# Kernel tuning notes

Hardware: AMD Instinct MI355X
Metric: run time of the kernel (lower is better)

## Reference

```python
import jax, jax.numpy as jnp
import numpy as np

DIM = 768
HEADS = 12
ROWS = COLS = 24          # 384 // 16
NP = ROWS * COLS          # 576 patches
N = NP + 1                # +1 cls token
NREL = (2 * ROWS - 1) * (2 * COLS - 1)  # 2209 relative offsets


def make_mapping_indices():
    # mapping[(di,dj)] = (di+ROWS-1)*(2*COLS-1) + (dj+COLS-1), vectorized
    i = np.arange(ROWS)[:, None, None, None]
    j = np.arange(COLS)[None, :, None, None]
    ii = np.arange(ROWS)[None, None, :, None]
    jj = np.arange(COLS)[None, None, None, :]
    idx = ((ii - i) + ROWS - 1) * (2 * COLS - 1) + ((jj - j) + COLS - 1)
    return jnp.asarray(idx.reshape(NP, NP), dtype=jnp.int32)


def setup_inputs() -> dict:
    key = jax.random.key(0)
    ks = jax.random.split(key, 7)
    B = 32
    x = jax.random.normal(ks[0], (B, N, DIM), dtype=jnp.float32)
    qkv_w = jax.random.normal(ks[1], (3 * DIM, DIM), dtype=jnp.float32) * 0.02
    proj_w = jax.random.normal(ks[2], (DIM, DIM), dtype=jnp.float32) * 0.02
    proj_b = jnp.zeros((DIM,), dtype=jnp.float32)
    beta1 = jax.random.normal(ks[3], (HEADS, 1, 1 + NP), dtype=jnp.float32) * 0.02
    beta2 = jax.random.normal(ks[4], (HEADS, NP, 1), dtype=jnp.float32) * 0.02
    beta3 = jax.random.normal(ks[5], (HEADS, NREL), dtype=jnp.float32) * 0.02
    return {"x": x, "qkv_w": qkv_w, "proj_w": proj_w, "proj_b": proj_b,
            "beta1": beta1, "beta2": beta2, "beta3": beta3,
            "mapping_indices": make_mapping_indices()}


def reference(x, qkv_w, proj_w, proj_b, beta1, beta2, beta3, mapping_indices):
    B, Nn, C = x.shape
    H = HEADS
    D = C // H
    scale = D ** -0.5
    qkv = x @ qkv_w.T                               # (B,N,3C)
    qkv = qkv.reshape(B, Nn, 3, H, D).transpose(2, 0, 3, 1, 4)
    q, k, v = qkv[0], qkv[1], qkv[2]                # (B,H,N,D)
    attn = jnp.einsum('bhid,bhjd->bhij', q, k) * scale
    # T5-style bias: (H, NP, NP) gathered rel bias + beta2 first col + beta1 last row
    rel = beta3[:, mapping_indices]                 # (H, NP, NP)
    top = jnp.concatenate([beta2, rel], axis=2)     # (H, NP, NP+1)
    beta_matrix = jnp.concatenate([top, beta1], axis=1)  # (H, N, N)
    attn = attn + beta_matrix[None]
    attn = jax.nn.softmax(attn, axis=-1)
    out = jnp.einsum('bhij,bhjd->bhid', attn, v)    # (B,H,N,D)
    out = out.transpose(0, 2, 1, 3).reshape(B, Nn, C)
    return out @ proj_w.T + proj_b
```

## Files before the change

kernel.cpp:

```cpp
#include <hip/hip_runtime.h>
#include <math.h>

#define DIMC  768
#define HEADS 12
#define NTOK  577
#define NPAT  576
#define NRELS 2209
#define BATCH 32
#define HDIM  64
#define MROWS (BATCH * NTOK)
#define NQB   5
#define NCH   10

#define AS1 __attribute__((address_space(1)))
#define AS3 __attribute__((address_space(3)))

typedef __attribute__((ext_vector_type(8))) short bf16x8;
typedef __attribute__((ext_vector_type(4))) float f32x4;
typedef __attribute__((ext_vector_type(8))) unsigned short u16x8;

__device__ __forceinline__ unsigned short f2bf(float f) {
    unsigned int u = __float_as_uint(f);
    return (unsigned short)((u + 0x7FFFu + ((u >> 16) & 1u)) >> 16);
}
__device__ __forceinline__ float bf2f(unsigned short h) {
    return __uint_as_float(((unsigned int)h) << 16);
}

__global__ __launch_bounds__(256)
void f32_to_bf16_kernel(const float* __restrict__ in, unsigned short* __restrict__ out, int n4) {
    for (int i = blockIdx.x * 256 + threadIdx.x; i < n4; i += gridDim.x * 256) {
        float4 v = reinterpret_cast<const float4*>(in)[i];
        ushort4 r;
        r.x = f2bf(v.x); r.y = f2bf(v.y); r.z = f2bf(v.z); r.w = f2bf(v.w);
        reinterpret_cast<ushort4*>(out)[i] = r;
    }
}

__global__ __launch_bounds__(256)
void build_biasF_kernel(const float* __restrict__ beta1,
                        const float* __restrict__ beta2,
                        const float* __restrict__ beta3,
                        unsigned short* __restrict__ biasF) {
    int idx = blockIdx.x * 256 + threadIdx.x;
    const int total = HEADS * NQB * NCH * 4 * 64 * 32;
    if (idx >= total) return;
    int r    = idx & 3;
    int bb   = (idx >> 2) & 3;
    int qi   = (idx >> 4) & 1;
    int lane = (idx >> 5) & 63;
    int wv   = (idx >> 11) & 3;
    int u    = idx >> 13;
    int c    = u % NCH;
    int i0b  = (u / NCH) % NQB;
    int h    = u / (NCH * NQB);
    int q = i0b * 128 + wv * 32 + qi * 16 + (lane & 15);
    int j = c * 64 + bb * 16 + ((lane >> 4) << 2) + r;
    float v;
    if (q >= NTOK || j >= NTOK) {
        v = -1e30f;
    } else if (q == NPAT) {
        v = beta1[h * NTOK + j];
    } else if (j == 0) {
        v = beta2[h * NPAT + q];
    } else {
        int p   = j - 1;
        int qi_ = q / 24, qj = q - qi_ * 24;
        int ri  = p / 24, ci = p - ri * 24;
        v = beta3[h * NRELS + (ri - qi_ + 23) * 47 + (ci - qj + 23)];
    }
    biasF[idx] = f2bf(v);
}

__global__ __launch_bounds__(256)
void vt_build_kernel(const unsigned short* __restrict__ qkv,
                     unsigned short* __restrict__ vtg) {
    __shared__ unsigned short T[64][72];
    const int c = blockIdx.x, h = blockIdx.y, b = blockIdx.z;
    const int tid = threadIdx.x;
    {
        int tok   = tid >> 2;
        int dq    = (tid & 3) << 4;
        int token = min(c * 64 + tok, NTOK - 1);
        const unsigned short* src = qkv + (size_t)(b * NTOK + token) * 2304 + 2 * DIMC + h * HDIM + dq;
        u16x8 a0 = *(const u16x8*)src;
        u16x8 a1 = *(const u16x8*)(src + 8);
        #pragma unroll
        for (int e = 0; e < 8; ++e) {
            T[dq + e][tok]     = (unsigned short)a0[e];
            T[dq + 8 + e][tok] = (unsigned short)a1[e];
        }
    }
    __syncthreads();
    {
        int d  = tid >> 2;
        int tq = (tid & 3) << 4;
        u16x8 r0 = *(const u16x8*)&T[d][tq];
        u16x8 r1 = *(const u16x8*)&T[d][tq + 8];
        unsigned short* dst = vtg + ((size_t)((b * HEADS + h) * HDIM) + d) * 640 + c * 64 + tq;
        *(u16x8*)dst       = r0;
        *(u16x8*)(dst + 8) = r1;
    }
}

template<bool ADD_BIAS, bool OUT_BF16, bool SCALE_Q>
__global__ __launch_bounds__(256, 2)
void gemm_128(const unsigned short* __restrict__ A,
              const unsigned short* __restrict__ B,
              const float* __restrict__ bias,
              void* __restrict__ Cv,
              int M, int N, int K, int Mb, int Nb) {
    __shared__ __align__(16) unsigned short As[2][128 * 64];
    __shared__ __align__(16) unsigned short Bs[2][128 * 64];
    const int tid  = threadIdx.x;
    const int w    = tid >> 6;
    const int lane = tid & 63;
    const int wm   = w >> 1, wn = w & 1;
    const int l15  = lane & 15, h4 = lane >> 4;

    const int nwg  = Mb * Nb;
    const int orig = blockIdx.x;
    const int qq   = nwg >> 3, rr8 = nwg & 7;
    const int xcd  = orig & 7, loc = orig >> 3;
    const int wgid = (xcd < rr8 ? xcd * (qq + 1) : rr8 * (qq + 1) + (xcd - rr8) * qq) + loc;
    const int nblk = wgid % Nb, mblk = wgid / Nb;
    const int m0 = mblk << 7, n0 = nblk << 7;

    const int r0 = tid >> 3;
    const int cs = (((tid & 7) ^ (r0 & 7)) << 3);
    const unsigned short* ap[4];
    const unsigned short* bp[4];
    #pragma unroll
    for (int g = 0; g < 4; ++g) {
        ap[g] = A + (size_t)min(m0 + g * 32 + r0, M - 1) * K + cs;
        bp[g] = B + (size_t)(n0 + g * 32 + r0) * K + cs;
    }

#define GLL(src, dst) __builtin_amdgcn_global_load_lds((const AS1 void*)(src), (AS3 void*)(dst), 16, 0, 0)
#define STAGE_TILE(t, buf)                                                  \
    {                                                                       \
        const int koff_ = (t) << 6;                                         \
        _Pragma("unroll")                                                   \
        for (int g = 0; g < 4; ++g) {                                       \
            GLL(ap[g] + koff_, &As[buf][(g * 256 + tid) * 8]);              \
            GLL(bp[g] + koff_, &Bs[buf][(g * 256 + tid) * 8]);              \
        }                                                                   \
    }

    f32x4 acc[4][4] = {};

    STAGE_TILE(0, 0);
    STAGE_TILE(1, 1);
    asm volatile("s_waitcnt vmcnt(8)" ::: "memory");
    __builtin_amdgcn_s_barrier();

    const int NT = K >> 6;
    for (int t = 0; t < NT; ++t) {
        const int buf = t & 1;
        bf16x8 af[2][4], bf[2][4];
        #pragma unroll
        for (int kb = 0; kb < 2; ++kb) {
            #pragma unroll
            for (int mf = 0; mf < 4; ++mf) {
                int row = wm * 64 + mf * 16 + l15;
                int ch  = (kb * 4 + h4) ^ (row & 7);
                af[kb][mf] = *(const bf16x8*)&As[buf][row * 64 + ch * 8];
            }
            #pragma unroll
            for (int nf = 0; nf < 4; ++nf) {
                int row = wn * 64 + nf * 16 + l15;
                int ch  = (kb * 4 + h4) ^ (row & 7);
                bf[kb][nf] = *(const bf16x8*)&Bs[buf][row * 64 + ch * 8];
            }
        }
        asm volatile("s_waitcnt lgkmcnt(0)" ::: "memory");
        __builtin_amdgcn_sched_barrier(0);
        __builtin_amdgcn_s_barrier();
        if (t + 2 < NT) STAGE_TILE(t + 2, buf);

        __builtin_amdgcn_s_setprio(1);
        #pragma unroll
        for (int kb = 0; kb < 2; ++kb)
            #pragma unroll
            for (int mf = 0; mf < 4; ++mf)
                #pragma unroll
                for (int nf = 0; nf < 4; ++nf)
                    acc[mf][nf] = __builtin_amdgcn_mfma_f32_16x16x32_bf16(
                        af[kb][mf], bf[kb][nf], acc[mf][nf], 0, 0, 0);
        __builtin_amdgcn_s_setprio(0);

        if (t + 2 < NT)
            asm volatile("s_waitcnt vmcnt(8)" ::: "memory");
        else if (t + 1 < NT)
            asm volatile("s_waitcnt vmcnt(0)" ::: "memory");
        __builtin_amdgcn_s_barrier();
    }
#undef STAGE_TILE
#undef GLL

    __builtin_amdgcn_s_barrier();
    float* scr = (float*)As + (w << 12);
    const int rowbase = m0 + wm * 64;
    const int colbase = n0 + wn * 64;
    #pragma unroll
    for (int mf = 0; mf < 4; ++mf)
        #pragma unroll
        for (int nf = 0; nf < 4; ++nf)
            #pragma unroll
            for (int r = 0; r < 4; ++r) {
                int row = mf * 16 + (h4 << 2) + r;
                int col = nf * 16 + l15;
                float v = acc[mf][nf][r];
                int gcol = colbase + col;
                if (ADD_BIAS) v += bias[gcol];
                if (SCALE_Q && gcol < DIMC) v *= 0.125f;
                scr[(row << 6) + (col ^ ((row & 7) << 3))] = v;
            }
    if (OUT_BF16) {
        const int rr = lane >> 3, c8 = (lane & 7) << 3;
        #pragma unroll
        for (int k8 = 0; k8 < 8; ++k8) {
            int row = k8 * 8 + rr;
            int p = (row << 6) + (c8 ^ ((row & 7) << 3));
            f32x4 v0 = *(const f32x4*)&scr[p];
            f32x4 v1 = *(const f32x4*)&scr[p + 4];
            int grow = rowbase + row;
            if (grow < M) {
                u16x8 o;
                o[0] = f2bf(v0[0]); o[1] = f2bf(v0[1]); o[2] = f2bf(v0[2]); o[3] = f2bf(v0[3]);
                o[4] = f2bf(v1[0]); o[5] = f2bf(v1[1]); o[6] = f2bf(v1[2]); o[7] = f2bf(v1[3]);
                *(u16x8*)((unsigned short*)Cv + (size_t)grow * N + colbase + c8) = o;
            }
        }
    } else {
        const int rr = lane >> 4, c4 = (lane & 15) << 2;
        #pragma unroll
        for (int k4 = 0; k4 < 16; ++k4) {
            int row = k4 * 4 + rr;
            f32x4 v = *(const f32x4*)&scr[(row << 6) + (c4 ^ ((row & 7) << 3))];
            int grow = rowbase + row;
            if (grow < M)
                *(f32x4*)((float*)Cv + (size_t)grow * N + colbase + c4) = v;
        }
    }
}

__global__ __launch_bounds__(256)
void attn_mfma2(const unsigned short* __restrict__ qkv,
                const unsigned short* __restrict__ vtg,
                const unsigned short* __restrict__ biasF,
                unsigned short* __restrict__ att) {
    __shared__ __align__(16) unsigned short Ks[64 * 64];
    __shared__ __align__(16) unsigned short Vs[64 * 64];
    __shared__ __align__(16) unsigned short Ps[128 * 64];

    const int b    = blockIdx.z;
    const int h    = blockIdx.y;
    const int i0b  = blockIdx.x;
    const int i0   = i0b << 7;
    const int tid  = threadIdx.x;
    const int w    = tid >> 6;
    const int lane = tid & 63;
    const int l15  = lane & 15;
    const int h4   = lane >> 4;
    const int sw   = (l15 & 7) << 3;

    bf16x8 qf[2][2];
    #pragma unroll
    for (int qi = 0; qi < 2; ++qi) {
        int qrow = min(i0 + w * 32 + qi * 16 + l15, NTOK - 1);
        const unsigned short* qp = qkv + (size_t)(b * NTOK + qrow) * 2304 + h * HDIM + h4 * 8;
        qf[qi][0] = *(const bf16x8*)qp;
        qf[qi][1] = *(const bf16x8*)(qp + 32);
    }

    const int grow   = lane >> 3;
    const int gchunk = (lane & 7) ^ grow;
    const unsigned short* kls = qkv + (size_t)b * NTOK * 2304 + DIMC + h * HDIM + gchunk * 8;
    const unsigned short* vls = vtg + (size_t)((b * HEADS + h) * HDIM) * 640 + gchunk * 8;
    const unsigned short* bias_p = biasF + ((size_t)(((h * NQB + i0b) * NCH) * 4 + w) * 64 + lane) * 32;

    float l[2] = {0.f, 0.f};
    f32x4 o[2][4] = {};

    for (int c = 0; c < NCH; ++c) {
        __syncthreads();
        #pragma unroll
        for (int t = 0; t < 2; ++t) {
            const int rbase = w * 16 + t * 8;
            const int rloc  = rbase + grow;
            const int ktok  = min(c * 64 + rloc, NTOK - 1);
            __builtin_amdgcn_global_load_lds((const AS1 void*)(kls + (size_t)ktok * 2304),
                                             (AS3 void*)(Ks + rbase * 64), 16, 0, 0);
            __builtin_amdgcn_global_load_lds((const AS1 void*)(vls + rloc * 640 + c * 64),
                                             (AS3 void*)(Vs + rbase * 64), 16, 0, 0);
        }
        u16x8 br[4];
        {
            const unsigned short* bp = bias_p + c * 8192;
            #pragma unroll
            for (int t = 0; t < 4; ++t) br[t] = *(const u16x8*)(bp + t * 8);
        }
        __syncthreads();

        __builtin_amdgcn_s_setprio(1);
        f32x4 sacc[4][2] = {};
        #pragma unroll
        for (int kb = 0; kb < 2; ++kb) {
            #pragma unroll
            for (int bb = 0; bb < 4; ++bb) {
                bf16x8 kf = *(const bf16x8*)&Ks[(bb * 16 + l15) * 64 + ((kb * 32 + h4 * 8) ^ sw)];
                sacc[bb][0] = __builtin_amdgcn_mfma_f32_16x16x32_bf16(kf, qf[0][kb], sacc[bb][0], 0, 0, 0);
                sacc[bb][1] = __builtin_amdgcn_mfma_f32_16x16x32_bf16(kf, qf[1][kb], sacc[bb][1], 0, 0, 0);
            }
        }
        __builtin_amdgcn_s_setprio(0);

        #pragma unroll
        for (int qi = 0; qi < 2; ++qi) {
            float rs = 0.f;
            #pragma unroll
            for (int bb = 0; bb < 4; ++bb) {
                const u16x8 bv = br[qi * 2 + (bb >> 1)];
                const int   e0 = (bb & 1) * 4;
                float p0 = __expf(sacc[bb][qi][0] + bf2f((unsigned short)bv[e0 + 0]));
                float p1 = __expf(sacc[bb][qi][1] + bf2f((unsigned short)bv[e0 + 1]));
                float p2 = __expf(sacc[bb][qi][2] + bf2f((unsigned short)bv[e0 + 2]));
                float p3 = __expf(sacc[bb][qi][3] + bf2f((unsigned short)bv[e0 + 3]));
                rs += (p0 + p1) + (p2 + p3);
                ushort4 pw;
                pw.x = f2bf(p0); pw.y = f2bf(p1); pw.z = f2bf(p2); pw.w = f2bf(p3);
                *(ushort4*)&Ps[(w * 32 + qi * 16 + l15) * 64 + ((bb * 16 + h4 * 4) ^ sw)] = pw;
            }
            rs += __shfl_xor(rs, 16);
            rs += __shfl_xor(rs, 32);
            l[qi] += rs;
        }

        __builtin_amdgcn_s_setprio(1);
        #pragma unroll
        for (int kb = 0; kb < 2; ++kb) {
            bf16x8 vf[4];
            #pragma unroll
            for (int nb = 0; nb < 4; ++nb)
                vf[nb] = *(const bf16x8*)&Vs[(nb * 16 + l15) * 64 + ((kb * 32 + h4 * 8) ^ sw)];
            #pragma unroll
            for (int qi = 0; qi < 2; ++qi) {
                bf16x8 pf = *(const bf16x8*)&Ps[(w * 32 + qi * 16 + l15) * 64 + ((kb * 32 + h4 * 8) ^ sw)];
                #pragma unroll
                for (int nb = 0; nb < 4; ++nb)
                    o[qi][nb] = __builtin_amdgcn_mfma_f32_16x16x32_bf16(pf, vf[nb], o[qi][nb], 0, 0, 0);
            }
        }
        __builtin_amdgcn_s_setprio(0);
    }

    #pragma unroll
    for (int qi = 0; qi < 2; ++qi) {
        #pragma unroll
        for (int r = 0; r < 4; ++r) {
            float linv = 1.0f / __shfl(l[qi], (h4 << 2) + r);
            int qrow = i0 + w * 32 + qi * 16 + (h4 << 2) + r;
            if (qrow < NTOK) {
                #pragma unroll
                for (int nb = 0; nb < 4; ++nb)
                    att[(size_t)(b * NTOK + qrow) * DIMC + h * HDIM + nb * 16 + l15] =
                        f2bf(o[qi][nb][r] * linv);
            }
        }
    }
}

extern "C" void kernel_launch(void* const* d_in, const int* in_sizes, int n_in,
                              void* d_out, int out_size, void* d_ws, size_t ws_size,
                              hipStream_t stream) {
    const float* x      = (const float*)d_in[0];
    const float* qkv_w  = (const float*)d_in[1];
    const float* proj_w = (const float*)d_in[2];
    const float* proj_b = (const float*)d_in[3];
    const float* beta1  = (const float*)d_in[4];
    const float* beta2  = (const float*)d_in[5];
    const float* beta3  = (const float*)d_in[6];
    float* out = (float*)d_out;

    unsigned short* qkvbf = (unsigned short*)d_ws;
    unsigned short* attbf = qkvbf + (size_t)MROWS * 2304;
    unsigned short* xbf   = attbf + (size_t)MROWS * DIMC;
    unsigned short* wqkv  = xbf   + (size_t)MROWS * DIMC;
    unsigned short* wproj = wqkv  + (size_t)2304 * DIMC;
    unsigned short* vtg   = wproj + (size_t)DIMC * DIMC;
    unsigned short* biasF = vtg   + (size_t)BATCH * HEADS * HDIM * 640;

    f32_to_bf16_kernel<<<2048, 256, 0, stream>>>(x, xbf, MROWS * DIMC / 4);
    f32_to_bf16_kernel<<<1024, 256, 0, stream>>>(qkv_w, wqkv, 2304 * DIMC / 4);
    f32_to_bf16_kernel<<<512, 256, 0, stream>>>(proj_w, wproj, DIMC * DIMC / 4);

    build_biasF_kernel<<<(HEADS * NQB * NCH * 4 * 64 * 32 + 255) / 256, 256, 0, stream>>>(
        beta1, beta2, beta3, biasF);

    {
        const int Mb = (MROWS + 127) / 128, Nb = (3 * DIMC) / 128;
        gemm_128<false, true, true><<<Mb * Nb, 256, 0, stream>>>(
            xbf, wqkv, nullptr, qkvbf, MROWS, 3 * DIMC, DIMC, Mb, Nb);
    }
    {
        dim3 g(NCH, HEADS, BATCH);
        vt_build_kernel<<<g, 256, 0, stream>>>(qkvbf, vtg);
    }
    {
        dim3 g(NQB, HEADS, BATCH);
        attn_mfma2<<<g, 256, 0, stream>>>(qkvbf, vtg, biasF, attbf);
    }
    {
        const int Mb = (MROWS + 127) / 128, Nb = DIMC / 128;
        gemm_128<true, false, false><<<Mb * Nb, 256, 0, stream>>>(
            attbf, wproj, proj_b, out, MROWS, DIMC, DIMC, Mb, Nb);
    }
}
```

Measured before the change: 355.1 us.

## Use exp2 softmax, packed bf16 convert, XCD-aware attention grid, fused casts

Folds log2(e) into the Q scale and the bias table so the softmax can use the native exp2 instruction instead of expf. Replaces the manual bf16 rounding of P with the packed v_cvt_pk_bf16_f32 instruction. Remaps the attention grid to 1D so that all query blocks of one (batch, head) land on the same XCD, which should improve L2 reuse of K/V. Merges the three fp32-to-bf16 conversion launches into one kernel to save launch overhead.

```diff
diff --git a/kernel.cpp b/kernel.cpp
--- a/kernel.cpp
+++ b/kernel.cpp
@@ -11,6 +11,8 @@
 #define MROWS (BATCH * NTOK)
 #define NQB   5
 #define NCH   10
+#define LOG2E 1.4426950408889634f
+#define QSC   (0.125f * LOG2E)
 
 #define AS1 __attribute__((address_space(1)))
 #define AS3 __attribute__((address_space(3)))
@@ -26,14 +28,26 @@
 __device__ __forceinline__ float bf2f(unsigned short h) {
     return __uint_as_float(((unsigned int)h) << 16);
 }
+__device__ __forceinline__ unsigned int cvt_pk_bf16(float lo, float hi) {
+    unsigned int r;
+    asm("v_cvt_pk_bf16_f32 %0, %1, %2" : "=v"(r) : "v"(lo), "v"(hi));
+    return r;
+}
 
 __global__ __launch_bounds__(256)
-void f32_to_bf16_kernel(const float* __restrict__ in, unsigned short* __restrict__ out, int n4) {
-    for (int i = blockIdx.x * 256 + threadIdx.x; i < n4; i += gridDim.x * 256) {
-        float4 v = reinterpret_cast<const float4*>(in)[i];
+void cvt3_kernel(const float* __restrict__ s1, unsigned short* __restrict__ d1, int n1,
+                 const float* __restrict__ s2, unsigned short* __restrict__ d2, int n2,
+                 const float* __restrict__ s3, unsigned short* __restrict__ d3, int n3) {
+    const int total = n1 + n2 + n3;
+    for (int i = blockIdx.x * 256 + threadIdx.x; i < total; i += gridDim.x * 256) {
+        const float* s; unsigned short* d; int k;
+        if (i < n1)            { s = s1; d = d1; k = i; }
+        else if (i < n1 + n2)  { s = s2; d = d2; k = i - n1; }
+        else                   { s = s3; d = d3; k = i - n1 - n2; }
+        float4 v = reinterpret_cast<const float4*>(s)[k];
         ushort4 r;
         r.x = f2bf(v.x); r.y = f2bf(v.y); r.z = f2bf(v.z); r.w = f2bf(v.w);
-        reinterpret_cast<ushort4*>(out)[i] = r;
+        reinterpret_cast<ushort4*>(d)[k] = r;
     }
 }
 
@@ -69,7 +83,7 @@
         int ri  = p / 24, ci = p - ri * 24;
         v = beta3[h * NRELS + (ri - qi_ + 23) * 47 + (ci - qj + 23)];
     }
-    biasF[idx] = f2bf(v);
+    biasF[idx] = f2bf(v * LOG2E);
 }
 
 __global__ __launch_bounds__(256)
@@ -213,7 +227,7 @@
                 float v = acc[mf][nf][r];
                 int gcol = colbase + col;
                 if (ADD_BIAS) v += bias[gcol];
-                if (SCALE_Q && gcol < DIMC) v *= 0.125f;
+                if (SCALE_Q && gcol < DIMC) v *= QSC;
                 scr[(row << 6) + (col ^ ((row & 7) << 3))] = v;
             }
     if (OUT_BF16) {
@@ -246,7 +260,7 @@
 }
 
 __global__ __launch_bounds__(256)
-void attn_mfma2(const unsigned short* __restrict__ qkv,
+void attn_mfma3(const unsigned short* __restrict__ qkv,
                 const unsigned short* __restrict__ vtg,
                 const unsigned short* __restrict__ biasF,
                 unsigned short* __restrict__ att) {
@@ -254,9 +268,15 @@
     __shared__ __align__(16) unsigned short Vs[64 * 64];
     __shared__ __align__(16) unsigned short Ps[128 * 64];
 
-    const int b    = blockIdx.z;
-    const int h    = blockIdx.y;
-    const int i0b  = blockIdx.x;
+    const int orig = blockIdx.x;
+    const int xcd  = orig & 7;
+    const int jj   = orig >> 3;
+    const int ul   = jj / 5;
+    const int i0b  = jj - ul * 5;
+    const int unit = xcd + (ul << 3);
+    const int h    = unit % HEADS;
+    const int b    = unit / HEADS;
+
     const int i0   = i0b << 7;
     const int tid  = threadIdx.x;
     const int w    = tid >> 6;
@@ -323,14 +343,15 @@
             for (int bb = 0; bb < 4; ++bb) {
                 const u16x8 bv = br[qi * 2 + (bb >> 1)];
                 const int   e0 = (bb & 1) * 4;
-                float p0 = __expf(sacc[bb][qi][0] + bf2f((unsigned short)bv[e0 + 0]));
-                float p1 = __expf(sacc[bb][qi][1] + bf2f((unsigned short)bv[e0 + 1]));
-                float p2 = __expf(sacc[bb][qi][2] + bf2f((unsigned short)bv[e0 + 2]));
-                float p3 = __expf(sacc[bb][qi][3] + bf2f((unsigned short)bv[e0 + 3]));
+                float p0 = __builtin_amdgcn_exp2f(sacc[bb][qi][0] + bf2f((unsigned short)bv[e0 + 0]));
+                float p1 = __builtin_amdgcn_exp2f(sacc[bb][qi][1] + bf2f((unsigned short)bv[e0 + 1]));
+                float p2 = __builtin_amdgcn_exp2f(sacc[bb][qi][2] + bf2f((unsigned short)bv[e0 + 2]));
+                float p3 = __builtin_amdgcn_exp2f(sacc[bb][qi][3] + bf2f((unsigned short)bv[e0 + 3]));
                 rs += (p0 + p1) + (p2 + p3);
-                ushort4 pw;
-                pw.x = f2bf(p0); pw.y = f2bf(p1); pw.z = f2bf(p2); pw.w = f2bf(p3);
-                *(ushort4*)&Ps[(w * 32 + qi * 16 + l15) * 64 + ((bb * 16 + h4 * 4) ^ sw)] = pw;
+                unsigned int u0 = cvt_pk_bf16(p0, p1);
+                unsigned int u1 = cvt_pk_bf16(p2, p3);
+                *(uint2*)&Ps[(w * 32 + qi * 16 + l15) * 64 + ((bb * 16 + h4 * 4) ^ sw)] =
+                    make_uint2(u0, u1);
             }
             rs += __shfl_xor(rs, 16);
             rs += __shfl_xor(rs, 32);
@@ -391,9 +412,9 @@
     unsigned short* vtg   = wproj + (size_t)DIMC * DIMC;
     unsigned short* biasF = vtg   + (size_t)BATCH * HEADS * HDIM * 640;
 
-    f32_to_bf16_kernel<<<2048, 256, 0, stream>>>(x, xbf, MROWS * DIMC / 4);
-    f32_to_bf16_kernel<<<1024, 256, 0, stream>>>(qkv_w, wqkv, 2304 * DIMC / 4);
-    f32_to_bf16_kernel<<<512, 256, 0, stream>>>(proj_w, wproj, DIMC * DIMC / 4);
+    cvt3_kernel<<<2048, 256, 0, stream>>>(x, xbf, MROWS * DIMC / 4,
+                                          qkv_w, wqkv, 2304 * DIMC / 4,
+                                          proj_w, wproj, DIMC * DIMC / 4);
 
     build_biasF_kernel<<<(HEADS * NQB * NCH * 4 * 64 * 32 + 255) / 256, 256, 0, stream>>>(
         beta1, beta2, beta3, biasF);
@@ -408,8 +429,7 @@
         vt_build_kernel<<<g, 256, 0, stream>>>(qkvbf, vtg);
     }
     {
-        dim3 g(NQB, HEADS, BATCH);
-        attn_mfma2<<<g, 256, 0, stream>>>(qkvbf, vtg, biasF, attbf);
+        attn_mfma3<<<NQB * HEADS * BATCH, 256, 0, stream>>>(qkvbf, vtg, biasF, attbf);
     }
     {
         const int Mb = (MROWS + 127) / 128, Nb = DIMC / 128;
```

New measurement: 329.2 us. 7.3% less time.
